# Optimization experiments

Measured on AMD Instinct MI355X. Metric: run time of the kernel, lower is better.

Reference implementation:

```python
import jax, jax.numpy as jnp
import numpy as np

# dims: N = inner-loop slices (only last used), T = tensorLen, M = matrixSize, A = aux feat, D = dense units
N, T, M, A, D = 4, 1024, 128, 64, 128
RELU = True


def setup_inputs() -> dict:
    key = jax.random.key(0)
    k1, k2, k3, k4 = jax.random.split(key, 4)
    x_main = jax.random.normal(k1, (N, T, 1, M, M), dtype=jnp.float32)
    x_aux = jax.random.normal(k2, (M, T, A), dtype=jnp.float32)
    W1 = jax.random.normal(k3, (A, D), dtype=jnp.float32) * 0.05
    b1 = jnp.zeros((D,), dtype=jnp.float32)
    W2 = jax.random.normal(k4, (D, M), dtype=jnp.float32) * 0.05
    b2 = jnp.zeros((M,), dtype=jnp.float32)
    return {"x_main": x_main, "x_aux": x_aux, "W1": W1, "b1": b1, "W2": W2, "b2": b2}


def reference(x_main, x_aux, W1, b1, W2, b2):
    # SLAM sublayer applied to every aux slice at once: [M, T, A] -> [M, T, M]
    h = jnp.einsum('mta,ad->mtd', x_aux, W1) + b1
    if RELU:
        h = jax.nn.relu(h)
    S = jnp.einsum('mtd,dk->mtk', h, W2) + b2  # SLAM(aux_slice_t) stacked over t
    # Original inner loop overwrites outer_product -> only the LAST main slice matters.
    main_last = x_main[-1, :, 0]  # [T, M, M] (squeeze of [1, M, M])
    out = jnp.einsum('tij,jtk->tik', main_last, S)  # per-slice matmul, stacked: [T, M, M]
    # expand_dims(-1) then expand_dims(0): [1, T, M, M, 1]
    return out[None, :, :, :, None]
```

## Files before the change

kernel.cpp:

```cpp
#include <hip/hip_runtime.h>


#define TT 1024
#define MM 128
#define AA 64
#define DD 128

typedef float  f32x4  __attribute__((ext_vector_type(4)));
typedef __bf16 bf16x8 __attribute__((ext_vector_type(8)));
typedef __bf16 bf16x4 __attribute__((ext_vector_type(4)));


__global__ __launch_bounds__(512, 1)
void slam_fused(const float* __restrict__ xm, const float* __restrict__ xa,
                const float* __restrict__ W1, const float* __restrict__ b1,
                const float* __restrict__ W2, const float* __restrict__ b2,
                float* __restrict__ out)
{
    __shared__ __bf16 ldsR1[18432];
    __shared__ __bf16 ldsH [17408];
    __shared__ __bf16 ldsW2[17408];
    __shared__ float  ldsB1[128];
    __shared__ float  ldsB2[128];

    const int t    = blockIdx.x;
    const int tid  = threadIdx.x;
    const int lane = tid & 63;
    const int wv   = tid >> 6;
    const int n    = lane & 15;
    const int q    = lane >> 4;

    __bf16* Xal  = ldsR1;
    __bf16* W1Tl = ldsR1 + 9216;
    __bf16* Sl   = ldsR1;

    const float* arow = xm + (size_t)3 * TT * MM * MM + ((size_t)t * MM + wv * 16 + n) * MM;
    f32x4 apre[8];
#pragma unroll
    for (int ks = 0; ks < 4; ++ks) {
        apre[2 * ks]     = *(const f32x4*)(arow + ks * 32 + q * 8);
        apre[2 * ks + 1] = *(const f32x4*)(arow + ks * 32 + q * 8 + 4);
    }

#pragma unroll
    for (int p = 0; p < 4; ++p) {
        int m = p * 32 + (tid >> 4);
        int c = (tid & 15) * 4;
        f32x4 v = *(const f32x4*)(xa + ((size_t)m * TT + t) * AA + c);
        bf16x4 pk;
        pk[0] = (__bf16)v[0]; pk[1] = (__bf16)v[1]; pk[2] = (__bf16)v[2]; pk[3] = (__bf16)v[3];
        *(bf16x4*)(Xal + m * 72 + c) = pk;
    }
#pragma unroll
    for (int p = 0; p < 4; ++p) {
        int idx = p * 512 + tid;
        int a = idx >> 5;
        int d = (idx & 31) * 4;
        f32x4 v = *(const f32x4*)(W1 + a * DD + d);
        W1Tl[(d + 0) * 72 + a] = (__bf16)v[0];
        W1Tl[(d + 1) * 72 + a] = (__bf16)v[1];
        W1Tl[(d + 2) * 72 + a] = (__bf16)v[2];
        W1Tl[(d + 3) * 72 + a] = (__bf16)v[3];
    }
#pragma unroll
    for (int p = 0; p < 8; ++p) {
        int idx = p * 512 + tid;
        int d = idx >> 5;
        int k = (idx & 31) * 4;
        f32x4 v = *(const f32x4*)(W2 + d * DD + k);
        ldsW2[(k + 0) * 136 + d] = (__bf16)v[0];
        ldsW2[(k + 1) * 136 + d] = (__bf16)v[1];
        ldsW2[(k + 2) * 136 + d] = (__bf16)v[2];
        ldsW2[(k + 3) * 136 + d] = (__bf16)v[3];
    }
    if (tid < 128)      ldsB1[tid] = b1[tid];
    else if (tid < 256) ldsB2[tid - 128] = b2[tid - 128];

    __syncthreads();

    f32x4 acc[8];

    {
        bf16x8 a1[2];
#pragma unroll
        for (int ks = 0; ks < 2; ++ks)
            a1[ks] = *(const bf16x8*)(W1Tl + (wv * 16 + n) * 72 + ks * 32 + q * 8);
#pragma unroll
        for (int mt = 0; mt < 8; ++mt) acc[mt] = (f32x4){0.f, 0.f, 0.f, 0.f};
#pragma unroll
        for (int mt = 0; mt < 8; ++mt) {
#pragma unroll
            for (int ks = 0; ks < 2; ++ks) {
                bf16x8 bb = *(const bf16x8*)(Xal + (mt * 16 + n) * 72 + ks * 32 + q * 8);
                acc[mt] = __builtin_amdgcn_mfma_f32_16x16x32_bf16(a1[ks], bb, acc[mt], 0, 0, 0);
            }
        }
        int dbase = wv * 16 + q * 4;
        float bv0 = ldsB1[dbase + 0], bv1 = ldsB1[dbase + 1];
        float bv2 = ldsB1[dbase + 2], bv3 = ldsB1[dbase + 3];
#pragma unroll
        for (int mt = 0; mt < 8; ++mt) {
            int m = mt * 16 + n;
            bf16x4 pk;
            pk[0] = (__bf16)fmaxf(acc[mt][0] + bv0, 0.f);
            pk[1] = (__bf16)fmaxf(acc[mt][1] + bv1, 0.f);
            pk[2] = (__bf16)fmaxf(acc[mt][2] + bv2, 0.f);
            pk[3] = (__bf16)fmaxf(acc[mt][3] + bv3, 0.f);
            *(bf16x4*)(ldsH + m * 136 + dbase) = pk;
        }
    }
    __syncthreads();

    {
        bf16x8 a2[4];
#pragma unroll
        for (int ks = 0; ks < 4; ++ks)
            a2[ks] = *(const bf16x8*)(ldsH + (wv * 16 + n) * 136 + ks * 32 + q * 8);
#pragma unroll
        for (int kt = 0; kt < 8; ++kt) acc[kt] = (f32x4){0.f, 0.f, 0.f, 0.f};
#pragma unroll
        for (int kt = 0; kt < 8; ++kt) {
#pragma unroll
            for (int ks = 0; ks < 4; ++ks) {
                bf16x8 bb = *(const bf16x8*)(ldsW2 + (kt * 16 + n) * 136 + ks * 32 + q * 8);
                acc[kt] = __builtin_amdgcn_mfma_f32_16x16x32_bf16(a2[ks], bb, acc[kt], 0, 0, 0);
            }
        }
        int jbase = wv * 16 + q * 4;
#pragma unroll
        for (int kt = 0; kt < 8; ++kt) {
            int k = kt * 16 + n;
            float bv = ldsB2[k];
            bf16x4 pk;
            pk[0] = (__bf16)(acc[kt][0] + bv);
            pk[1] = (__bf16)(acc[kt][1] + bv);
            pk[2] = (__bf16)(acc[kt][2] + bv);
            pk[3] = (__bf16)(acc[kt][3] + bv);
            *(bf16x4*)(Sl + k * 136 + jbase) = pk;
        }
    }
    __syncthreads();

    {
        bf16x8 a3[4];
#pragma unroll
        for (int ks = 0; ks < 4; ++ks) {
            f32x4 lo = apre[2 * ks], hi = apre[2 * ks + 1];
            bf16x8 v;
            v[0] = (__bf16)lo[0]; v[1] = (__bf16)lo[1]; v[2] = (__bf16)lo[2]; v[3] = (__bf16)lo[3];
            v[4] = (__bf16)hi[0]; v[5] = (__bf16)hi[1]; v[6] = (__bf16)hi[2]; v[7] = (__bf16)hi[3];
            a3[ks] = v;
        }
#pragma unroll
        for (int kt = 0; kt < 8; ++kt) acc[kt] = (f32x4){0.f, 0.f, 0.f, 0.f};
#pragma unroll
        for (int kt = 0; kt < 8; ++kt) {
#pragma unroll
            for (int ks = 0; ks < 4; ++ks) {
                bf16x8 bb = *(const bf16x8*)(Sl + (kt * 16 + n) * 136 + ks * 32 + q * 8);
                acc[kt] = __builtin_amdgcn_mfma_f32_16x16x32_bf16(a3[ks], bb, acc[kt], 0, 0, 0);
            }
        }
        float* orow = out + (size_t)t * MM * MM;
        int ibase = wv * 16 + q * 4;
#pragma unroll
        for (int kt = 0; kt < 8; ++kt) {
            int k = kt * 16 + n;
#pragma unroll
            for (int r = 0; r < 4; ++r)
                orow[(size_t)(ibase + r) * MM + k] = acc[kt][r];
        }
    }
}

extern "C" void kernel_launch(void* const* d_in, const int* in_sizes, int n_in,
                              void* d_out, int out_size, void* d_ws, size_t ws_size,
                              hipStream_t stream) {
    const float* xm = (const float*)d_in[0];
    const float* xa = (const float*)d_in[1];
    const float* W1 = (const float*)d_in[2];
    const float* b1 = (const float*)d_in[3];
    const float* W2 = (const float*)d_in[4];
    const float* b2 = (const float*)d_in[5];
    float* out = (float*)d_out;
    slam_fused<<<dim3(TT), dim3(512), 0, stream>>>(xm, xa, W1, b1, W2, b2, out);
}
```

Baseline: 370.1 us.

## Precompute bf16 transposed weights in a prep kernel and shrink LDS

Adds a small prep kernel that converts W1 and W2 to transposed bf16 in workspace once per call. The main kernel then reads weight fragments straight from global/L2 instead of staging and transposing them through LDS in every block. This cuts LDS from about 106KB to about 70KB and raises the launch-bounds occupancy hint. It adds a second launch and uncoalesced global weight reads in the MFMA loops. The main-slice bf16 conversion also moves earlier, which raises register pressure.

```diff
diff --git a/kernel.cpp b/kernel.cpp
--- a/kernel.cpp
+++ b/kernel.cpp
@@ -10,16 +10,29 @@
 typedef __bf16 bf16x8 __attribute__((ext_vector_type(8)));
 typedef __bf16 bf16x4 __attribute__((ext_vector_type(4)));
 
+__global__ __launch_bounds__(512, 1)
+void slam_prep(const float* __restrict__ W1, const float* __restrict__ W2,
+               __bf16* __restrict__ ws)
+{
+    int idx = blockIdx.x * 512 + threadIdx.x;
+    if (idx < DD * AA) {
+        int d = idx >> 6, a = idx & 63;
+        ws[idx] = (__bf16)W1[a * DD + d];
+    } else {
+        int i2 = idx - DD * AA;
+        int k = i2 >> 7, d = i2 & 127;
+        ws[DD * AA + i2] = (__bf16)W2[d * MM + k];
+    }
+}
 
-__global__ __launch_bounds__(512, 1)
+__global__ __launch_bounds__(512, 4)
 void slam_fused(const float* __restrict__ xm, const float* __restrict__ xa,
-                const float* __restrict__ W1, const float* __restrict__ b1,
-                const float* __restrict__ W2, const float* __restrict__ b2,
+                const float* __restrict__ b1, const float* __restrict__ b2,
+                const __bf16* __restrict__ wsW1T, const __bf16* __restrict__ wsW2T,
                 float* __restrict__ out)
 {
-    __shared__ __bf16 ldsR1[18432];
-    __shared__ __bf16 ldsH [17408];
-    __shared__ __bf16 ldsW2[17408];
+    __shared__ __bf16 ldsA[17408];
+    __shared__ __bf16 ldsH[17408];
     __shared__ float  ldsB1[128];
     __shared__ float  ldsB2[128];
 
@@ -30,16 +43,16 @@
     const int n    = lane & 15;
     const int q    = lane >> 4;
 
-    __bf16* Xal  = ldsR1;
-    __bf16* W1Tl = ldsR1 + 9216;
-    __bf16* Sl   = ldsR1;
-
     const float* arow = xm + (size_t)3 * TT * MM * MM + ((size_t)t * MM + wv * 16 + n) * MM;
-    f32x4 apre[8];
+    bf16x8 a3[4];
 #pragma unroll
     for (int ks = 0; ks < 4; ++ks) {
-        apre[2 * ks]     = *(const f32x4*)(arow + ks * 32 + q * 8);
-        apre[2 * ks + 1] = *(const f32x4*)(arow + ks * 32 + q * 8 + 4);
+        f32x4 lo = *(const f32x4*)(arow + ks * 32 + q * 8);
+        f32x4 hi = *(const f32x4*)(arow + ks * 32 + q * 8 + 4);
+        bf16x8 v;
+        v[0] = (__bf16)lo[0]; v[1] = (__bf16)lo[1]; v[2] = (__bf16)lo[2]; v[3] = (__bf16)lo[3];
+        v[4] = (__bf16)hi[0]; v[5] = (__bf16)hi[1]; v[6] = (__bf16)hi[2]; v[7] = (__bf16)hi[3];
+        a3[ks] = v;
     }
 
 #pragma unroll
@@ -49,29 +62,7 @@
         f32x4 v = *(const f32x4*)(xa + ((size_t)m * TT + t) * AA + c);
         bf16x4 pk;
         pk[0] = (__bf16)v[0]; pk[1] = (__bf16)v[1]; pk[2] = (__bf16)v[2]; pk[3] = (__bf16)v[3];
-        *(bf16x4*)(Xal + m * 72 + c) = pk;
-    }
-#pragma unroll
-    for (int p = 0; p < 4; ++p) {
-        int idx = p * 512 + tid;
-        int a = idx >> 5;
-        int d = (idx & 31) * 4;
-        f32x4 v = *(const f32x4*)(W1 + a * DD + d);
-        W1Tl[(d + 0) * 72 + a] = (__bf16)v[0];
-        W1Tl[(d + 1) * 72 + a] = (__bf16)v[1];
-        W1Tl[(d + 2) * 72 + a] = (__bf16)v[2];
-        W1Tl[(d + 3) * 72 + a] = (__bf16)v[3];
-    }
-#pragma unroll
-    for (int p = 0; p < 8; ++p) {
-        int idx = p * 512 + tid;
-        int d = idx >> 5;
-        int k = (idx & 31) * 4;
-        f32x4 v = *(const f32x4*)(W2 + d * DD + k);
-        ldsW2[(k + 0) * 136 + d] = (__bf16)v[0];
-        ldsW2[(k + 1) * 136 + d] = (__bf16)v[1];
-        ldsW2[(k + 2) * 136 + d] = (__bf16)v[2];
-        ldsW2[(k + 3) * 136 + d] = (__bf16)v[3];
+        *(bf16x4*)(ldsA + m * 72 + c) = pk;
     }
     if (tid < 128)      ldsB1[tid] = b1[tid];
     else if (tid < 256) ldsB2[tid - 128] = b2[tid - 128];
@@ -81,17 +72,17 @@
     f32x4 acc[8];
 
     {
+        const __bf16* w1r = wsW1T + (wv * 16 + n) * AA;
         bf16x8 a1[2];
-#pragma unroll
-        for (int ks = 0; ks < 2; ++ks)
-            a1[ks] = *(const bf16x8*)(W1Tl + (wv * 16 + n) * 72 + ks * 32 + q * 8);
+        a1[0] = *(const bf16x8*)(w1r + q * 8);
+        a1[1] = *(const bf16x8*)(w1r + 32 + q * 8);
 #pragma unroll
         for (int mt = 0; mt < 8; ++mt) acc[mt] = (f32x4){0.f, 0.f, 0.f, 0.f};
 #pragma unroll
         for (int mt = 0; mt < 8; ++mt) {
 #pragma unroll
             for (int ks = 0; ks < 2; ++ks) {
-                bf16x8 bb = *(const bf16x8*)(Xal + (mt * 16 + n) * 72 + ks * 32 + q * 8);
+                bf16x8 bb = *(const bf16x8*)(ldsA + (mt * 16 + n) * 72 + ks * 32 + q * 8);
                 acc[mt] = __builtin_amdgcn_mfma_f32_16x16x32_bf16(a1[ks], bb, acc[mt], 0, 0, 0);
             }
         }
@@ -120,9 +111,10 @@
         for (int kt = 0; kt < 8; ++kt) acc[kt] = (f32x4){0.f, 0.f, 0.f, 0.f};
 #pragma unroll
         for (int kt = 0; kt < 8; ++kt) {
+            const __bf16* w2r = wsW2T + (kt * 16 + n) * DD + q * 8;
 #pragma unroll
             for (int ks = 0; ks < 4; ++ks) {
-                bf16x8 bb = *(const bf16x8*)(ldsW2 + (kt * 16 + n) * 136 + ks * 32 + q * 8);
+                bf16x8 bb = *(const bf16x8*)(w2r + ks * 32);
                 acc[kt] = __builtin_amdgcn_mfma_f32_16x16x32_bf16(a2[ks], bb, acc[kt], 0, 0, 0);
             }
         }
@@ -136,28 +128,19 @@
             pk[1] = (__bf16)(acc[kt][1] + bv);
             pk[2] = (__bf16)(acc[kt][2] + bv);
             pk[3] = (__bf16)(acc[kt][3] + bv);
-            *(bf16x4*)(Sl + k * 136 + jbase) = pk;
+            *(bf16x4*)(ldsA + k * 136 + jbase) = pk;
         }
     }
     __syncthreads();
 
     {
-        bf16x8 a3[4];
-#pragma unroll
-        for (int ks = 0; ks < 4; ++ks) {
-            f32x4 lo = apre[2 * ks], hi = apre[2 * ks + 1];
-            bf16x8 v;
-            v[0] = (__bf16)lo[0]; v[1] = (__bf16)lo[1]; v[2] = (__bf16)lo[2]; v[3] = (__bf16)lo[3];
-            v[4] = (__bf16)hi[0]; v[5] = (__bf16)hi[1]; v[6] = (__bf16)hi[2]; v[7] = (__bf16)hi[3];
-            a3[ks] = v;
-        }
 #pragma unroll
         for (int kt = 0; kt < 8; ++kt) acc[kt] = (f32x4){0.f, 0.f, 0.f, 0.f};
 #pragma unroll
         for (int kt = 0; kt < 8; ++kt) {
 #pragma unroll
             for (int ks = 0; ks < 4; ++ks) {
-                bf16x8 bb = *(const bf16x8*)(Sl + (kt * 16 + n) * 136 + ks * 32 + q * 8);
+                bf16x8 bb = *(const bf16x8*)(ldsA + (kt * 16 + n) * 136 + ks * 32 + q * 8);
                 acc[kt] = __builtin_amdgcn_mfma_f32_16x16x32_bf16(a3[ks], bb, acc[kt], 0, 0, 0);
             }
         }
@@ -183,5 +166,10 @@
     const float* W2 = (const float*)d_in[4];
     const float* b2 = (const float*)d_in[5];
     float* out = (float*)d_out;
-    slam_fused<<<dim3(TT), dim3(512), 0, stream>>>(xm, xa, W1, b1, W2, b2, out);
+
+    __bf16* wsW1T = (__bf16*)d_ws;
+    __bf16* wsW2T = wsW1T + DD * AA;
+
+    slam_prep<<<dim3(48), dim3(512), 0, stream>>>(W1, W2, wsW1T);
+    slam_fused<<<dim3(TT), dim3(512), 0, stream>>>(xm, xa, b1, b2, wsW1T, wsW2T, out);
 }
```

Measured after the change: 381.9 us. +3.2%, slower.
